# Performance work log

Hardware: AMD Instinct MI355X
Metric: run time of the kernel (lower is better)

The kernel has to match this reference:

```python
import jax, jax.numpy as jnp
import numpy as np

INP, HID = 32, 64
NG, NPER = 16, 16384          # graphs, nodes per graph (contiguous, equal size)
N = NG * NPER                 # 262144 nodes
E = N * 16                    # 4194304 edges
K = 7                         # topk
STEPS = 5                     # future prediction heads
P0, P1 = INP * HID, HID * HID # GRU hidden sizes = GCN weight numel per layer
EPS = 1e-5


def setup_inputs() -> dict:
    key = jax.random.key(0)
    ks = jax.random.split(key, 32)
    s = 0.05
    inp = {
        "x": jax.random.normal(ks[0], (N, INP), jnp.float32),
        "edge_index": jax.random.randint(ks[1], (2, E), 0, N),
        "edge_weight": jax.random.uniform(ks[2], (E,), jnp.float32),
        "batch": jnp.arange(N) // NPER,
        "batch_size": NG,
        # summarization score vectors p per layer
        "p0": jax.random.normal(ks[3], (INP,), jnp.float32),
        "p1": jax.random.normal(ks[4], (HID,), jnp.float32),
        # GRUCell params, layer 0: input INP -> hidden P0
        "Wih0": jax.random.normal(ks[5], (3 * P0, INP), jnp.float32) * s,
        "Whh0": jax.random.normal(ks[6], (3 * P0, P0), jnp.float32) * s,
        "bih0": jnp.zeros((3 * P0,), jnp.float32),
        "bhh0": jnp.zeros((3 * P0,), jnp.float32),
        # GRUCell params, layer 1: input HID -> hidden P1
        "Wih1": jax.random.normal(ks[7], (3 * P1, HID), jnp.float32) * s,
        "Whh1": jax.random.normal(ks[8], (3 * P1, P1), jnp.float32) * s,
        "bih1": jnp.zeros((3 * P1,), jnp.float32),
        "bhh1": jnp.zeros((3 * P1,), jnp.float32),
        # GRU hidden states (persistent buffers), one row per graph in batch
        "gruh0": jax.random.normal(ks[9], (NG, P0), jnp.float32) * s,
        "gruh1": jax.random.normal(ks[10], (NG, P1), jnp.float32) * s,
        # GCN biases (weights come from evolved GRU hidden)
        "gcnb0": jnp.zeros((HID,), jnp.float32),
        "gcnb1": jnp.zeros((HID,), jnp.float32),
        # LayerNorm params
        "lng0": jnp.ones((HID,), jnp.float32),
        "lnb0": jnp.zeros((HID,), jnp.float32),
        "lng1": jnp.ones((HID,), jnp.float32),
        "lnb1": jnp.zeros((HID,), jnp.float32),
        # 5 future-predictor heads Linear(HID, 2), stacked
        "Wp": jax.random.normal(ks[11], (STEPS, HID, 2), jnp.float32) * s,
        "bp": jnp.zeros((STEPS, 2), jnp.float32),
    }
    return inp


def _summarize(h, B, k, p):
    # per-graph topk summarization: score = h @ p/||p||, weight topk rows by tanh(score), mean
    d = h.shape[-1]
    hg = h.reshape(B, -1, d)                          # [B, Nper, d]
    scores = hg @ (p / jnp.linalg.norm(p))            # [B, Nper]
    top_s, idx = jax.lax.top_k(scores, k)             # [B, k]
    top_h = jnp.take_along_axis(hg, idx[:, :, None], axis=1)  # [B, k, d]
    return (top_h * jnp.tanh(top_s)[:, :, None]).mean(axis=1)  # [B, d]


def _gru_cell(x, h, Wih, Whh, bih, bhh):
    gi = x @ Wih.T + bih
    gh = h @ Whh.T + bhh
    i_r, i_z, i_n = jnp.split(gi, 3, axis=-1)
    h_r, h_z, h_n = jnp.split(gh, 3, axis=-1)
    r = jax.nn.sigmoid(i_r + h_r)
    z = jax.nn.sigmoid(i_z + h_z)
    n = jnp.tanh(i_n + r * h_n)
    return (1.0 - z) * n + z * h


def _gcn_conv(h, W, b, src, dst, ew, n_nodes):
    # GCNConv with self-loops (weight 1) and symmetric normalization
    x = h @ W + b                                     # linear first (PyG order)
    deg = jnp.zeros((n_nodes,), x.dtype).at[dst].add(ew) + 1.0
    norm = ew * jax.lax.rsqrt(deg[src] * deg[dst])
    out = jnp.zeros_like(x).at[dst].add(norm[:, None] * x[src])
    return out + x / deg[:, None]                     # self-loop: 1/deg_i


def _layer_norm(h, g, b):
    mu = h.mean(-1, keepdims=True)
    var = ((h - mu) ** 2).mean(-1, keepdims=True)
    return (h - mu) * jax.lax.rsqrt(var + EPS) * g + b


def reference(x, edge_index, edge_weight, batch, batch_size,
              p0, p1, Wih0, Whh0, bih0, bhh0, Wih1, Whh1, bih1, bhh1,
              gruh0, gruh1, gcnb0, gcnb1, lng0, lnb0, lng1, lnb1, Wp, bp):
    src, dst = edge_index[0], edge_index[1]
    n_nodes = x.shape[0]
    layers = [
        (p0, Wih0, Whh0, bih0, bhh0, gruh0, gcnb0, lng0, lnb0, (INP, HID)),
        (p1, Wih1, Whh1, bih1, bhh1, gruh1, gcnb1, lng1, lnb1, (HID, HID)),
    ]
    h = x
    for (p, Wih, Whh, bih, bhh, gh, gb, lg, lb, (din, dout)) in layers:
        Z = _summarize(h, batch_size, K, p)                # [B, din]
        gh_new = _gru_cell(Z, gh, Wih, Whh, bih, bhh)      # [B, din*dout]
        W = gh_new.mean(axis=0).reshape(din, dout)         # evolved GCN weight
        h = _gcn_conv(h, W, gb, src, dst, edge_weight, n_nodes)
        h = jax.nn.relu(_layer_norm(h, lg, lb))            # dropout: eval mode (identity)
    # stacked prediction heads -> [N, STEPS, 2]
    return jnp.einsum("nd,sdo->nso", h, Wp) + bp[None, :, :]
```

## Files before the change

### kernel.cpp

```cpp
#include <hip/hip_runtime.h>
#include <hip/hip_bf16.h>
#include <hip/hip_fp16.h>

#define NN 262144
#define EE 4194304
#define NG 16
#define NPER 16384
#define KK 7
#define TPAD 20
#define SLOT 18432

typedef unsigned long long u64;

__device__ __forceinline__ float wred(float v) {
    #pragma unroll
    for (int o = 32; o > 0; o >>= 1) v += __shfl_xor(v, o);
    return v;
}

__device__ __forceinline__ unsigned short f2h(float f) {
    return __half_as_ushort(__float2half_rn(f));
}
__device__ __forceinline__ float h2f(unsigned short s) {
    return __half2float(__ushort_as_half(s));
}

__global__ void prep_p(const float* __restrict__ p0, const float* __restrict__ p1,
                       float* __restrict__ pn) {
    int t = threadIdx.x;
    float v0 = (t < 32) ? p0[t] : 0.f;
    float s0 = wred(v0 * v0);
    if (t < 32) pn[t] = v0 * rsqrtf(s0);
    float v1 = p1[t];
    float s1 = wred(v1 * v1);
    pn[32 + t] = v1 * rsqrtf(s1);
}

__global__ void init_gcur(int* __restrict__ gcur) {
    gcur[threadIdx.x] = (int)threadIdx.x * SLOT;
}

__global__ __launch_bounds__(256) void binA(const int* __restrict__ ei,
                                            const float* __restrict__ ew,
                                            int* __restrict__ gcur,
                                            uint2* __restrict__ bb) {
    __shared__ int hist[256], hofs[256], hcur[256], gpos[256], sd[256];
    __shared__ uint2 stage[4096];
    int t = threadIdx.x;
    int base = blockIdx.x * 4096;
    hist[t] = 0;
    __syncthreads();
    int dv[16];
    #pragma unroll
    for (int j = 0; j < 16; j++) {
        dv[j] = ei[EE + base + j * 256 + t];
        atomicAdd(&hist[dv[j] >> 10], 1);
    }
    __syncthreads();
    int cnt = hist[t];
    sd[t] = cnt;
    __syncthreads();
    #pragma unroll
    for (int off = 1; off < 256; off <<= 1) {
        int add = (t >= off) ? sd[t - off] : 0;
        __syncthreads();
        sd[t] += add;
        __syncthreads();
    }
    hofs[t] = sd[t] - cnt;
    hcur[t] = sd[t] - cnt;
    gpos[t] = atomicAdd(&gcur[t], cnt);
    __syncthreads();
    #pragma unroll
    for (int j = 0; j < 16; j++) {
        int e = base + j * 256 + t;
        int d = dv[j];
        int s = ei[e];
        unsigned wq = (unsigned)__float2uint_rn(ew[e] * 16383.f);
        unsigned payload = ((unsigned)s << 14) | wq;
        int p = atomicAdd(&hcur[d >> 10], 1);
        stage[p] = make_uint2((unsigned)d, payload);
    }
    __syncthreads();
    #pragma unroll
    for (int j = 0; j < 16; j++) {
        int k = j * 256 + t;
        uint2 en = stage[k];
        int b = (int)(en.x >> 10);
        bb[gpos[b] + (k - hofs[b])] = en;
    }
}

__global__ __launch_bounds__(1024) void count_bucket(const uint2* __restrict__ bb,
                                                     const int* __restrict__ gcur,
                                                     int* __restrict__ rowptr,
                                                     int* __restrict__ btot,
                                                     float* __restrict__ rsqd,
                                                     float* __restrict__ invdeg) {
    __shared__ int cnt[1024];
    __shared__ int wsi[1024];
    __shared__ int sd[1024];
    int b = blockIdx.x, t = threadIdx.x;
    cnt[t] = 0;
    wsi[t] = 0;
    __syncthreads();
    int e0 = b * SLOT, e1 = gcur[b];
    for (int k = e0 + t; k < e1; k += 1024) {
        uint2 en = bb[k];
        int dl = (int)(en.x & 1023u);
        atomicAdd(&cnt[dl], 1);
        atomicAdd(&wsi[dl], (int)(en.y & 16383u));
    }
    __syncthreads();
    int node = (b << 10) + t;
    float deg = 1.f + (float)wsi[t] * (1.f / 16383.f);
    rsqd[node] = rsqrtf(deg);
    invdeg[node] = 1.f / deg;
    int v = cnt[t];
    sd[t] = v;
    __syncthreads();
    #pragma unroll
    for (int off = 1; off < 1024; off <<= 1) {
        int add = (t >= off) ? sd[t - off] : 0;
        __syncthreads();
        sd[t] += add;
        __syncthreads();
    }
    rowptr[node] = sd[t] - v;
    if (t == 1023) btot[b] = sd[1023];
}

__global__ void scan256(const int* __restrict__ btot, int* __restrict__ bbase) {
    __shared__ int sd[256];
    int t = threadIdx.x;
    int v = btot[t];
    sd[t] = v;
    __syncthreads();
    #pragma unroll
    for (int off = 1; off < 256; off <<= 1) {
        int add = (t >= off) ? sd[t - off] : 0;
        __syncthreads();
        sd[t] += add;
        __syncthreads();
    }
    bbase[t] = sd[t] - v;
}

__global__ void finalize_rowptr(int* __restrict__ rowptr, const int* __restrict__ bbase) {
    int i = blockIdx.x * 256 + threadIdx.x;
    rowptr[i] += bbase[i >> 10];
    if (i == 0) rowptr[NN] = EE;
}

__global__ __launch_bounds__(1024) void binB(const int* __restrict__ rowptr,
                                             const int* __restrict__ gcur,
                                             const uint2* __restrict__ bb,
                                             const float* __restrict__ rsqd,
                                             unsigned* __restrict__ evw) {
    __shared__ int lcur[1024];
    int b = blockIdx.x, t = threadIdx.x;
    lcur[t] = rowptr[(b << 10) + t];
    __syncthreads();
    int e0 = b * SLOT, e1 = gcur[b];
    for (int k = e0 + t; k < e1; k += 1024) {
        uint2 en = bb[k];
        int dl = (int)(en.x & 1023u);
        unsigned s = en.y >> 14;
        float wt = (float)(en.y & 16383u) * (1.f / 16383.f) * rsqd[s];
        int pos = atomicAdd(&lcur[dl], 1);
        evw[pos] = (s << 14) | (unsigned)__float2uint_rn(wt * 16383.f);
    }
}

__global__ void scores0_f16(const float* __restrict__ x, const float* __restrict__ pn0,
                            float* __restrict__ scores, unsigned short* __restrict__ xh) {
    __shared__ float p[32];
    if (threadIdx.x < 32) p[threadIdx.x] = pn0[threadIdx.x];
    __syncthreads();
    int n = blockIdx.x * 256 + threadIdx.x;
    const float4* xr = (const float4*)(x + (size_t)n * 32);
    float s = 0.f;
    unsigned wv[16];
    #pragma unroll
    for (int j = 0; j < 8; j++) {
        float4 v = xr[j];
        s += v.x * p[j * 4] + v.y * p[j * 4 + 1] + v.z * p[j * 4 + 2] + v.w * p[j * 4 + 3];
        wv[2 * j]     = (unsigned)f2h(v.x) | ((unsigned)f2h(v.y) << 16);
        wv[2 * j + 1] = (unsigned)f2h(v.z) | ((unsigned)f2h(v.w) << 16);
    }
    uint4* xo = (uint4*)(xh + (size_t)n * 32);
    xo[0] = make_uint4(wv[0], wv[1], wv[2], wv[3]);
    xo[1] = make_uint4(wv[4], wv[5], wv[6], wv[7]);
    xo[2] = make_uint4(wv[8], wv[9], wv[10], wv[11]);
    xo[3] = make_uint4(wv[12], wv[13], wv[14], wv[15]);
    scores[n] = s;
}

__global__ void topk1(const float* __restrict__ scores, float2* __restrict__ cand) {
    int g = blockIdx.x >> 4, c = blockIdx.x & 15;
    int t = threadIdx.x;
    float lv[KK];
    int li[KK];
    #pragma unroll
    for (int j = 0; j < KK; j++) { lv[j] = -INFINITY; li[j] = 0; }
    const float* sg = scores + (size_t)g * NPER + c * 1024;
    #pragma unroll
    for (int it = 0; it < 4; ++it) {
        int idx = it * 256 + t;
        float v = sg[idx];
        if (v > lv[KK - 1]) {
            int j = KK - 1;
            while (j > 0 && lv[j - 1] < v) { lv[j] = lv[j - 1]; li[j] = li[j - 1]; j--; }
            lv[j] = v; li[j] = idx;
        }
    }
    __shared__ float sval[256];
    __shared__ int sidx[256];
    __shared__ int swin;
    int cons = 0;
    for (int r = 0; r < KK; r++) {
        sval[t] = (cons < KK) ? lv[cons] : -INFINITY;
        sidx[t] = t;
        __syncthreads();
        for (int s = 128; s > 0; s >>= 1) {
            if (t < s) {
                if (sval[t + s] > sval[t]) { sval[t] = sval[t + s]; sidx[t] = sidx[t + s]; }
            }
            __syncthreads();
        }
        if (t == 0) swin = sidx[0];
        __syncthreads();
        if (t == swin) {
            cand[blockIdx.x * KK + r] =
                make_float2(lv[cons], __int_as_float(g * NPER + c * 1024 + li[cons]));
            cons++;
        }
        __syncthreads();
    }
}

__global__ void topk2(const float2* __restrict__ cand, float* __restrict__ topv,
                      int* __restrict__ topi) {
    int g = blockIdx.x, t = threadIdx.x;
    float v = -INFINITY;
    int id = 0;
    if (t < 16 * KK) {
        float2 cv = cand[g * 16 * KK + t];
        v = cv.x;
        id = __float_as_int(cv.y);
    }
    __shared__ float sval[128];
    __shared__ int sidx[128];
    __shared__ int swin;
    for (int r = 0; r < KK; r++) {
        sval[t] = v;
        sidx[t] = t;
        __syncthreads();
        for (int s = 64; s > 0; s >>= 1) {
            if (t < s) {
                if (sval[t + s] > sval[t]) { sval[t] = sval[t + s]; sidx[t] = sidx[t + s]; }
            }
            __syncthreads();
        }
        if (t == 0) swin = sidx[0];
        __syncthreads();
        if (t == swin) {
            topv[g * KK + r] = v;
            topi[g * KK + r] = id;
            v = -INFINITY;
        }
        __syncthreads();
    }
}

__global__ void z_kernel(const float* __restrict__ h, int din, const float* __restrict__ topv,
                         const int* __restrict__ topi, float* __restrict__ Z) {
    int b = blockIdx.x;
    int d = threadIdx.x;
    if (d >= din) return;
    float acc = 0.f;
    for (int j = 0; j < KK; j++) {
        acc += tanhf(topv[b * KK + j]) * h[(size_t)topi[b * KK + j] * din + d];
    }
    Z[b * din + d] = acc * (1.f / 7.f);
}

__global__ void z_kernel_h(const unsigned short* __restrict__ h, int din,
                           const float* __restrict__ topv, const int* __restrict__ topi,
                           float* __restrict__ Z) {
    int b = blockIdx.x;
    int d = threadIdx.x;
    if (d >= din) return;
    float acc = 0.f;
    for (int j = 0; j < KK; j++) {
        acc += tanhf(topv[b * KK + j]) * h2f(h[(size_t)topi[b * KK + j] * din + d]);
    }
    Z[b * din + d] = acc * (1.f / 7.f);
}

__global__ void gru_matvec(const float* __restrict__ Whh, const float* __restrict__ gh,
                           float* __restrict__ ghl, int P) {
    int t = threadIdx.x;
    int g = t >> 4, l16 = t & 15;
    int row0 = blockIdx.x * 64 + g * 4;
    int k0 = blockIdx.y * 512;
    float acc[4][16];
    #pragma unroll
    for (int r = 0; r < 4; r++)
        #pragma unroll
        for (int b = 0; b < 16; b++) acc[r][b] = 0.f;
    const float* wr = Whh + (size_t)row0 * P + k0 + l16 * 4;
    const float* gr = gh + k0 + l16 * 4;
    for (int kk = 0; kk < 8; ++kk) {
        float4 a0 = *(const float4*)(wr + kk * 64);
        float4 a1 = *(const float4*)(wr + (size_t)P + kk * 64);
        float4 a2 = *(const float4*)(wr + (size_t)2 * P + kk * 64);
        float4 a3 = *(const float4*)(wr + (size_t)3 * P + kk * 64);
        #pragma unroll
        for (int b = 0; b < 16; b++) {
            float4 gv = *(const float4*)(gr + (size_t)b * P + kk * 64);
            acc[0][b] += a0.x * gv.x + a0.y * gv.y + a0.z * gv.z + a0.w * gv.w;
            acc[1][b] += a1.x * gv.x + a1.y * gv.y + a1.z * gv.z + a1.w * gv.w;
            acc[2][b] += a2.x * gv.x + a2.y * gv.y + a2.z * gv.z + a2.w * gv.w;
            acc[3][b] += a3.x * gv.x + a3.y * gv.y + a3.z * gv.z + a3.w * gv.w;
        }
    }
    size_t sstr = (size_t)gridDim.x * 1024;
    #pragma unroll
    for (int r = 0; r < 4; r++) {
        #pragma unroll
        for (int b = 0; b < 16; b++) {
            float v = acc[r][b];
            v += __shfl_xor(v, 1); v += __shfl_xor(v, 2);
            v += __shfl_xor(v, 4); v += __shfl_xor(v, 8);
            if (l16 == b) ghl[(size_t)blockIdx.y * sstr + (size_t)(row0 + r) * 16 + b] = v;
        }
    }
}

__global__ __launch_bounds__(256) void gate_kernel(
    const float* __restrict__ Wih, const float* __restrict__ bih,
    const float* __restrict__ bhh, const float* __restrict__ gh,
    const float* __restrict__ ghl, const float* __restrict__ Zg,
    float* __restrict__ gvt, int P, int din, int NS) {
    __shared__ float Zs[64];
    int t = threadIdx.x;
    int b = blockIdx.y;
    if (t < din) Zs[t] = Zg[b * din + t];
    __syncthreads();
    int p = blockIdx.x * 256 + t;
    float ir = bih[p], iz = bih[P + p], inn = bih[2 * P + p];
    const float* w_r = Wih + (size_t)p * din;
    const float* w_z = Wih + (size_t)(P + p) * din;
    const float* w_n = Wih + (size_t)(2 * P + p) * din;
    for (int d = 0; d < din; d += 4) {
        float4 zr = *(const float4*)(Zs + d);
        float4 a = *(const float4*)(w_r + d);
        float4 bq = *(const float4*)(w_z + d);
        float4 c = *(const float4*)(w_n + d);
        ir += a.x * zr.x + a.y * zr.y + a.z * zr.z + a.w * zr.w;
        iz += bq.x * zr.x + bq.y * zr.y + bq.z * zr.z + bq.w * zr.w;
        inn += c.x * zr.x + c.y * zr.y + c.z * zr.z + c.w * zr.w;
    }
    float hr = bhh[p], hz = bhh[P + p], hn = bhh[2 * P + p];
    size_t sstr = (size_t)48 * P;
    for (int s2 = 0; s2 < NS; s2++) {
        const float* g2 = ghl + (size_t)s2 * sstr;
        hr += g2[(size_t)p * 16 + b];
        hz += g2[(size_t)(P + p) * 16 + b];
        hn += g2[(size_t)(2 * P + p) * 16 + b];
    }
    float r = 1.f / (1.f + expf(-(ir + hr)));
    float z = 1.f / (1.f + expf(-(iz + hz)));
    float n = tanhf(inn + r * hn);
    float hprev = gh[(size_t)b * P + p];
    gvt[(size_t)b * P + p] = (1.f - z) * n + z * hprev;
}

__global__ void gate_reduce(const float* __restrict__ gvt, float* __restrict__ Wev, int P) {
    int p = blockIdx.x * 256 + threadIdx.x;
    float s = 0.f;
    #pragma unroll
    for (int b = 0; b < 16; b++) s += gvt[(size_t)b * P + p];
    Wev[p] = s * (1.f / 16.f);
}

template<int DIN, int LSHL>
__global__ void agg_kernel(const unsigned short* __restrict__ hin,
                           const int* __restrict__ rowptr, const unsigned* __restrict__ evw,
                           const float* __restrict__ rsqd, const float* __restrict__ invdeg,
                           unsigned short* __restrict__ aggh, float* __restrict__ cc) {
    int t = threadIdx.x;
    int lane = t & ((1 << LSHL) - 1);
    int i = blockIdx.x * (256 >> LSHL) + (t >> LSHL);
    int e0 = rowptr[i], e1 = rowptr[i + 1];
    float a0 = 0.f, a1 = 0.f, a2 = 0.f, a3 = 0.f;
    int csi = 0;
    for (int e = e0; e < e1; e += 8) {
        unsigned ev[8];
        #pragma unroll
        for (int j = 0; j < 8; j++) {
            ev[j] = (e + j < e1) ? evw[e + j] : ((unsigned)i << 14);
        }
        uint2 hv[8];
        #pragma unroll
        for (int j = 0; j < 8; j++) {
            hv[j] = *(const uint2*)(hin + (size_t)(ev[j] >> 14) * DIN + 4 * lane);
        }
        #pragma unroll
        for (int j = 0; j < 8; j++) {
            int wq = (int)(ev[j] & 16383u);
            csi += wq;
            float nw = (float)wq;
            a0 += nw * h2f((unsigned short)(hv[j].x & 0xffffu));
            a1 += nw * h2f((unsigned short)(hv[j].x >> 16));
            a2 += nw * h2f((unsigned short)(hv[j].y & 0xffffu));
            a3 += nw * h2f((unsigned short)(hv[j].y >> 16));
        }
    }
    float rsi = rsqd[i] * (1.f / 16383.f);
    float idg = invdeg[i];
    uint2 hs = *(const uint2*)(hin + (size_t)i * DIN + 4 * lane);
    float r0 = a0 * rsi + h2f((unsigned short)(hs.x & 0xffffu)) * idg;
    float r1 = a1 * rsi + h2f((unsigned short)(hs.x >> 16)) * idg;
    float r2 = a2 * rsi + h2f((unsigned short)(hs.y & 0xffffu)) * idg;
    float r3 = a3 * rsi + h2f((unsigned short)(hs.y >> 16)) * idg;
    uint2 ro;
    ro.x = (unsigned)f2h(r0) | ((unsigned)f2h(r1) << 16);
    ro.y = (unsigned)f2h(r2) | ((unsigned)f2h(r3) << 16);
    *(uint2*)(aggh + (size_t)i * DIN + 4 * lane) = ro;
    #pragma unroll
    for (int o = (1 << LSHL) >> 1; o > 0; o >>= 1) csi += __shfl_xor(csi, o);
    if (lane == 0) cc[i] = (float)csi * rsi + idg;
}

__global__ __launch_bounds__(256) void post0_kernel(
    const unsigned short* __restrict__ aggh, const float* __restrict__ cc,
    const float* __restrict__ Wev, const float* __restrict__ gcnb,
    const float* __restrict__ lng, const float* __restrict__ lnb,
    const float* __restrict__ pn1, unsigned short* __restrict__ h1h,
    float* __restrict__ scores) {
    __shared__ float stage[4][512];
    __shared__ float tile[4][64 * TPAD];
    const int wv = threadIdx.x >> 6;
    const int lane = threadIdx.x & 63;
    const int tb = blockIdx.x * 256 + wv * 64;
    const int j = lane & 15, q = lane >> 4;
    float gL = gcnb[lane];
    float lgv[16], lbv[16], pnv[16];
    #pragma unroll
    for (int r = 0; r < 16; r++) {
        lgv[r] = lng[q * 16 + r];
        lbv[r] = lnb[q * 16 + r];
        pnv[r] = pn1[q * 16 + r];
    }
    float* st = stage[wv];
    float* trow = tile[wv] + lane * TPAD;
    auto do_chunk = [&](int C) {
        __syncthreads();
        {
            const uint2* src = (const uint2*)(aggh + (size_t)(tb + C * 16) * 32);
            #pragma unroll
            for (int it = 0; it < 2; ++it) {
                uint2 hp = src[it * 64 + lane];
                float4 f;
                f.x = h2f((unsigned short)(hp.x & 0xffffu));
                f.y = h2f((unsigned short)(hp.x >> 16));
                f.z = h2f((unsigned short)(hp.y & 0xffffu));
                f.w = h2f((unsigned short)(hp.y >> 16));
                *(float4*)(st + (it * 64 + lane) * 4) = f;
            }
        }
        __syncthreads();
        float v[16];
        #pragma unroll
        for (int k = 0; k < 16; k++) v[k] = 0.f;
        for (int db = 0; db < 8; ++db) {
            float wc0 = Wev[(db * 4 + 0) * 64 + lane];
            float wc1 = Wev[(db * 4 + 1) * 64 + lane];
            float wc2 = Wev[(db * 4 + 2) * 64 + lane];
            float wc3 = Wev[(db * 4 + 3) * 64 + lane];
            #pragma unroll
            for (int k = 0; k < 16; k++) {
                float4 a = *(const float4*)(st + k * 32 + db * 4);
                v[k] += a.x * wc0 + a.y * wc1 + a.z * wc2 + a.w * wc3;
            }
        }
        __syncthreads();
        #pragma unroll
        for (int k = 0; k < 16; k++) trow[k] = v[k] + gL * cc[tb + C * 16 + k];
        __syncthreads();
        float av[16];
        #pragma unroll
        for (int r = 0; r < 16; r++) av[r] = tile[wv][(q * 16 + r) * TPAD + j];
        float s1 = 0.f, s2 = 0.f;
        #pragma unroll
        for (int r = 0; r < 16; r++) { s1 += av[r]; s2 += av[r] * av[r]; }
        s1 += __shfl_xor(s1, 16); s1 += __shfl_xor(s1, 32);
        s2 += __shfl_xor(s2, 16); s2 += __shfl_xor(s2, 32);
        float mu = s1 * (1.f / 64.f);
        float rstd = rsqrtf(s2 * (1.f / 64.f) - mu * mu + 1e-5f);
        float hv[16];
        float sc = 0.f;
        #pragma unroll
        for (int r = 0; r < 16; r++) {
            hv[r] = fmaxf((av[r] - mu) * rstd * lgv[r] + lbv[r], 0.f);
            sc += hv[r] * pnv[r];
        }
        int node = tb + C * 16 + j;
        uint4 o0, o1;
        o0.x = (unsigned)f2h(hv[0])  | ((unsigned)f2h(hv[1])  << 16);
        o0.y = (unsigned)f2h(hv[2])  | ((unsigned)f2h(hv[3])  << 16);
        o0.z = (unsigned)f2h(hv[4])  | ((unsigned)f2h(hv[5])  << 16);
        o0.w = (unsigned)f2h(hv[6])  | ((unsigned)f2h(hv[7])  << 16);
        o1.x = (unsigned)f2h(hv[8])  | ((unsigned)f2h(hv[9])  << 16);
        o1.y = (unsigned)f2h(hv[10]) | ((unsigned)f2h(hv[11]) << 16);
        o1.z = (unsigned)f2h(hv[12]) | ((unsigned)f2h(hv[13]) << 16);
        o1.w = (unsigned)f2h(hv[14]) | ((unsigned)f2h(hv[15]) << 16);
        *(uint4*)(h1h + (size_t)node * 64 + q * 16) = o0;
        *(uint4*)(h1h + (size_t)node * 64 + q * 16 + 8) = o1;
        sc += __shfl_xor(sc, 16); sc += __shfl_xor(sc, 32);
        if (q == 0) scores[node] = sc;
    };
    do_chunk(0); do_chunk(1); do_chunk(2); do_chunk(3);
}

__global__ __launch_bounds__(256) void post1_kernel(
    const unsigned short* __restrict__ aggh, const float* __restrict__ cc,
    const float* __restrict__ Wev, const float* __restrict__ gcnb,
    const float* __restrict__ lng, const float* __restrict__ lnb,
    const float* __restrict__ Wp, const float* __restrict__ bp,
    float* __restrict__ out) {
    __shared__ float stage[4][1024];
    __shared__ float tile[4][64 * TPAD];
    const int wv = threadIdx.x >> 6;
    const int lane = threadIdx.x & 63;
    const int tb = blockIdx.x * 256 + wv * 64;
    const int j = lane & 15, q = lane >> 4;
    float gL = gcnb[lane];
    float lgv[16], lbv[16];
    #pragma unroll
    for (int r = 0; r < 16; r++) {
        lgv[r] = lng[q * 16 + r];
        lbv[r] = lnb[q * 16 + r];
    }
    float bpv[10];
    #pragma unroll
    for (int t2 = 0; t2 < 10; t2++) bpv[t2] = bp[t2];
    float* st = stage[wv];
    float* trow = tile[wv] + lane * TPAD;
    auto do_chunk = [&](int C) {
        __syncthreads();
        {
            const uint2* src = (const uint2*)(aggh + (size_t)(tb + C * 16) * 64);
            #pragma unroll
            for (int it = 0; it < 4; ++it) {
                uint2 hp = src[it * 64 + lane];
                float4 f;
                f.x = h2f((unsigned short)(hp.x & 0xffffu));
                f.y = h2f((unsigned short)(hp.x >> 16));
                f.z = h2f((unsigned short)(hp.y & 0xffffu));
                f.w = h2f((unsigned short)(hp.y >> 16));
                *(float4*)(st + (it * 64 + lane) * 4) = f;
            }
        }
        __syncthreads();
        float v[16];
        #pragma unroll
        for (int k = 0; k < 16; k++) v[k] = 0.f;
        for (int db = 0; db < 16; ++db) {
            float wc0 = Wev[(db * 4 + 0) * 64 + lane];
            float wc1 = Wev[(db * 4 + 1) * 64 + lane];
            float wc2 = Wev[(db * 4 + 2) * 64 + lane];
            float wc3 = Wev[(db * 4 + 3) * 64 + lane];
            #pragma unroll
            for (int k = 0; k < 16; k++) {
                float4 a = *(const float4*)(st + k * 64 + db * 4);
                v[k] += a.x * wc0 + a.y * wc1 + a.z * wc2 + a.w * wc3;
            }
        }
        __syncthreads();
        #pragma unroll
        for (int k = 0; k < 16; k++) trow[k] = v[k] + gL * cc[tb + C * 16 + k];
        __syncthreads();
        float av[16];
        #pragma unroll
        for (int r = 0; r < 16; r++) av[r] = tile[wv][(q * 16 + r) * TPAD + j];
        float s1 = 0.f, s2 = 0.f;
        #pragma unroll
        for (int r = 0; r < 16; r++) { s1 += av[r]; s2 += av[r] * av[r]; }
        s1 += __shfl_xor(s1, 16); s1 += __shfl_xor(s1, 32);
        s2 += __shfl_xor(s2, 16); s2 += __shfl_xor(s2, 32);
        float mu = s1 * (1.f / 64.f);
        float rstd = rsqrtf(s2 * (1.f / 64.f) - mu * mu + 1e-5f);
        float hv[16];
        #pragma unroll
        for (int r = 0; r < 16; r++)
            hv[r] = fmaxf((av[r] - mu) * rstd * lgv[r] + lbv[r], 0.f);
        float oa[10];
        #pragma unroll
        for (int t2 = 0; t2 < 10; t2++) oa[t2] = 0.f;
        #pragma unroll
        for (int r = 0; r < 16; r++) {
            const float* wpb = Wp + (size_t)(q * 16 + r) * 2;
            float2 w0 = *(const float2*)(wpb);
            float2 w1 = *(const float2*)(wpb + 128);
            float2 w2 = *(const float2*)(wpb + 256);
            float2 w3 = *(const float2*)(wpb + 384);
            float2 w4 = *(const float2*)(wpb + 512);
            oa[0] += hv[r] * w0.x; oa[1] += hv[r] * w0.y;
            oa[2] += hv[r] * w1.x; oa[3] += hv[r] * w1.y;
            oa[4] += hv[r] * w2.x; oa[5] += hv[r] * w2.y;
            oa[6] += hv[r] * w3.x; oa[7] += hv[r] * w3.y;
            oa[8] += hv[r] * w4.x; oa[9] += hv[r] * w4.y;
        }
        #pragma unroll
        for (int t2 = 0; t2 < 10; t2++) {
            oa[t2] += __shfl_xor(oa[t2], 16);
            oa[t2] += __shfl_xor(oa[t2], 32);
        }
        if (q == 0) {
            int node = tb + C * 16 + j;
            #pragma unroll
            for (int t2 = 0; t2 < 10; t2++) out[(size_t)node * 10 + t2] = oa[t2] + bpv[t2];
        }
    };
    do_chunk(0); do_chunk(1); do_chunk(2); do_chunk(3);
}

extern "C" void kernel_launch(void* const* d_in, const int* in_sizes, int n_in,
                              void* d_out, int out_size, void* d_ws, size_t ws_size,
                              hipStream_t stream) {
    const float* x     = (const float*)d_in[0];
    const int*   ei    = (const int*)d_in[1];
    const float* ew    = (const float*)d_in[2];
    const float* p0    = (const float*)d_in[5];
    const float* p1    = (const float*)d_in[6];
    const float* Wih0  = (const float*)d_in[7];
    const float* Whh0  = (const float*)d_in[8];
    const float* bih0  = (const float*)d_in[9];
    const float* bhh0  = (const float*)d_in[10];
    const float* Wih1  = (const float*)d_in[11];
    const float* Whh1  = (const float*)d_in[12];
    const float* bih1  = (const float*)d_in[13];
    const float* bhh1  = (const float*)d_in[14];
    const float* gruh0 = (const float*)d_in[15];
    const float* gruh1 = (const float*)d_in[16];
    const float* gcnb0 = (const float*)d_in[17];
    const float* gcnb1 = (const float*)d_in[18];
    const float* lng0  = (const float*)d_in[19];
    const float* lnb0  = (const float*)d_in[20];
    const float* lng1  = (const float*)d_in[21];
    const float* lnb1  = (const float*)d_in[22];
    const float* Wp    = (const float*)d_in[23];
    const float* bp    = (const float*)d_in[24];
    float* out = (float*)d_out;

    char* w = (char*)d_ws;
    size_t off = 0;
    auto alloc = [&](size_t bytes) -> void* {
        void* p = w + off;
        off += (bytes + 255) & ~(size_t)255;
        return p;
    };
    int*      rowptr = (int*)alloc((NN + 1) * sizeof(int));
    unsigned* evw    = (unsigned*)alloc((size_t)EE * sizeof(unsigned));
    float*    rsqd   = (float*)alloc(NN * sizeof(float));
    float*    invdeg = (float*)alloc(NN * sizeof(float));
    float*    scores = (float*)alloc(NN * sizeof(float));
    float*    topv   = (float*)alloc(NG * KK * sizeof(float));
    int*      topi   = (int*)alloc(NG * KK * sizeof(int));
    float2*   cand   = (float2*)alloc(NG * 16 * KK * sizeof(float2));
    float*    Z      = (float*)alloc(16 * 64 * sizeof(float));
    float*    ghl    = (float*)alloc((size_t)8 * 196608 * sizeof(float));
    float*    gvt    = (float*)alloc((size_t)16 * 4096 * sizeof(float));
    float*    Wev    = (float*)alloc(4096 * sizeof(float));
    float*    cc     = (float*)alloc(NN * sizeof(float));
    float*    agg    = (float*)alloc((size_t)NN * 64 * sizeof(float));
    unsigned short* xh  = (unsigned short*)alloc((size_t)NN * 32 * sizeof(unsigned short));
    unsigned short* h1h = (unsigned short*)alloc((size_t)NN * 64 * sizeof(unsigned short));
    float*    pn     = (float*)alloc(96 * sizeof(float));
    int*      gcur   = (int*)alloc(256 * sizeof(int));
    int*      btot   = (int*)alloc(256 * sizeof(int));
    int*      bbase  = (int*)alloc(256 * sizeof(int));

    uint2* bb = (uint2*)agg;
    unsigned short* aggh = (unsigned short*)agg;

    init_gcur<<<1, 256, 0, stream>>>(gcur);
    prep_p<<<1, 64, 0, stream>>>(p0, p1, pn);
    binA<<<EE / 4096, 256, 0, stream>>>(ei, ew, gcur, bb);
    count_bucket<<<256, 1024, 0, stream>>>(bb, gcur, rowptr, btot, rsqd, invdeg);
    scan256<<<1, 256, 0, stream>>>(btot, bbase);
    finalize_rowptr<<<NN / 256, 256, 0, stream>>>(rowptr, bbase);
    binB<<<256, 1024, 0, stream>>>(rowptr, gcur, bb, rsqd, evw);

    scores0_f16<<<NN / 256, 256, 0, stream>>>(x, pn, scores, xh);
    topk1<<<NG * 16, 256, 0, stream>>>(scores, cand);
    topk2<<<NG, 128, 0, stream>>>(cand, topv, topi);
    z_kernel<<<NG, 32, 0, stream>>>(x, 32, topv, topi, Z);
    gru_matvec<<<dim3(6144 / 64, 4), 256, 0, stream>>>(Whh0, gruh0, ghl, 2048);
    gate_kernel<<<dim3(2048 / 256, 16), 256, 0, stream>>>(Wih0, bih0, bhh0, gruh0, ghl, Z, gvt, 2048, 32, 4);
    gate_reduce<<<2048 / 256, 256, 0, stream>>>(gvt, Wev, 2048);
    agg_kernel<32, 3><<<NN / 32, 256, 0, stream>>>(xh, rowptr, evw, rsqd, invdeg, aggh, cc);
    post0_kernel<<<NN / 256, 256, 0, stream>>>(aggh, cc, Wev, gcnb0, lng0, lnb0, pn + 32, h1h, scores);

    topk1<<<NG * 16, 256, 0, stream>>>(scores, cand);
    topk2<<<NG, 128, 0, stream>>>(cand, topv, topi);
    z_kernel_h<<<NG, 64, 0, stream>>>(h1h, 64, topv, topi, Z);
    gru_matvec<<<dim3(12288 / 64, 8), 256, 0, stream>>>(Whh1, gruh1, ghl, 4096);
    gate_kernel<<<dim3(4096 / 256, 16), 256, 0, stream>>>(Wih1, bih1, bhh1, gruh1, ghl, Z, gvt, 4096, 64, 8);
    gate_reduce<<<4096 / 256, 256, 0, stream>>>(gvt, Wev, 4096);
    agg_kernel<64, 4><<<NN / 16, 256, 0, stream>>>(h1h, rowptr, evw, rsqd, invdeg, aggh, cc);
    post1_kernel<<<NN / 256, 256, 0, stream>>>(aggh, cc, Wev, gcnb1, lng1, lnb1, Wp, bp, out);
}
```

Before: 634.8 us.

## Fuse small kernels: scores with topk1, topk2 with Z, init with prep

Merges init_gcur and prep_p into one launch, fuses layer-0 score computation and fp16 conversion with the first topk stage so scores are never written, and fuses topk2 with the Z gather for both layers. It also switches the bucket reads in count_bucket and binB to nontemporal 64-bit loads. The goal is to cut kernel-launch overhead and one score round-trip through memory. In exchange, scores0_topk1 runs only 256 blocks, each doing four times more work, so it exposes less parallelism for the x read.

```diff
diff --git a/kernel.cpp b/kernel.cpp
--- a/kernel.cpp
+++ b/kernel.cpp
@@ -25,19 +25,18 @@
     return __half2float(__ushort_as_half(s));
 }
 
-__global__ void prep_p(const float* __restrict__ p0, const float* __restrict__ p1,
-                       float* __restrict__ pn) {
+__global__ void prep_init(const float* __restrict__ p0, const float* __restrict__ p1,
+                          float* __restrict__ pn, int* __restrict__ gcur) {
     int t = threadIdx.x;
-    float v0 = (t < 32) ? p0[t] : 0.f;
-    float s0 = wred(v0 * v0);
-    if (t < 32) pn[t] = v0 * rsqrtf(s0);
-    float v1 = p1[t];
-    float s1 = wred(v1 * v1);
-    pn[32 + t] = v1 * rsqrtf(s1);
-}
-
-__global__ void init_gcur(int* __restrict__ gcur) {
-    gcur[threadIdx.x] = (int)threadIdx.x * SLOT;
+    gcur[t] = t * SLOT;
+    if (t < 64) {
+        float v0 = (t < 32) ? p0[t] : 0.f;
+        float s0 = wred(v0 * v0);
+        if (t < 32) pn[t] = v0 * rsqrtf(s0);
+        float v1 = p1[t];
+        float s1 = wred(v1 * v1);
+        pn[32 + t] = v1 * rsqrtf(s1);
+    }
 }
 
 __global__ __launch_bounds__(256) void binA(const int* __restrict__ ei,
@@ -106,10 +105,12 @@
     __syncthreads();
     int e0 = b * SLOT, e1 = gcur[b];
     for (int k = e0 + t; k < e1; k += 1024) {
-        uint2 en = bb[k];
-        int dl = (int)(en.x & 1023u);
+        u64 raw = __builtin_nontemporal_load((const u64*)(bb + k));
+        unsigned lo = (unsigned)raw;
+        unsigned hi = (unsigned)(raw >> 32);
+        int dl = (int)(lo & 1023u);
         atomicAdd(&cnt[dl], 1);
-        atomicAdd(&wsi[dl], (int)(en.y & 16383u));
+        atomicAdd(&wsi[dl], (int)(hi & 16383u));
     }
     __syncthreads();
     int node = (b << 10) + t;
@@ -163,47 +164,85 @@
     __syncthreads();
     int e0 = b * SLOT, e1 = gcur[b];
     for (int k = e0 + t; k < e1; k += 1024) {
-        uint2 en = bb[k];
-        int dl = (int)(en.x & 1023u);
-        unsigned s = en.y >> 14;
-        float wt = (float)(en.y & 16383u) * (1.f / 16383.f) * rsqd[s];
+        u64 raw = __builtin_nontemporal_load((const u64*)(bb + k));
+        unsigned lo = (unsigned)raw;
+        unsigned hi = (unsigned)(raw >> 32);
+        int dl = (int)(lo & 1023u);
+        unsigned s = hi >> 14;
+        float wt = (float)(hi & 16383u) * (1.f / 16383.f) * rsqd[s];
         int pos = atomicAdd(&lcur[dl], 1);
         evw[pos] = (s << 14) | (unsigned)__float2uint_rn(wt * 16383.f);
     }
 }
 
-__global__ void scores0_f16(const float* __restrict__ x, const float* __restrict__ pn0,
-                            float* __restrict__ scores, unsigned short* __restrict__ xh) {
+__global__ __launch_bounds__(256) void scores0_topk1(
+    const float* __restrict__ x, const float* __restrict__ pn0,
+    unsigned short* __restrict__ xh, float2* __restrict__ cand) {
     __shared__ float p[32];
     if (threadIdx.x < 32) p[threadIdx.x] = pn0[threadIdx.x];
     __syncthreads();
-    int n = blockIdx.x * 256 + threadIdx.x;
-    const float4* xr = (const float4*)(x + (size_t)n * 32);
-    float s = 0.f;
-    unsigned wv[16];
-    #pragma unroll
-    for (int j = 0; j < 8; j++) {
-        float4 v = xr[j];
-        s += v.x * p[j * 4] + v.y * p[j * 4 + 1] + v.z * p[j * 4 + 2] + v.w * p[j * 4 + 3];
-        wv[2 * j]     = (unsigned)f2h(v.x) | ((unsigned)f2h(v.y) << 16);
-        wv[2 * j + 1] = (unsigned)f2h(v.z) | ((unsigned)f2h(v.w) << 16);
-    }
-    uint4* xo = (uint4*)(xh + (size_t)n * 32);
-    xo[0] = make_uint4(wv[0], wv[1], wv[2], wv[3]);
-    xo[1] = make_uint4(wv[4], wv[5], wv[6], wv[7]);
-    xo[2] = make_uint4(wv[8], wv[9], wv[10], wv[11]);
-    xo[3] = make_uint4(wv[12], wv[13], wv[14], wv[15]);
-    scores[n] = s;
-}
-
-__global__ void topk1(const float* __restrict__ scores, float2* __restrict__ cand) {
-    int g = blockIdx.x >> 4, c = blockIdx.x & 15;
     int t = threadIdx.x;
     float lv[KK];
     int li[KK];
     #pragma unroll
     for (int j = 0; j < KK; j++) { lv[j] = -INFINITY; li[j] = 0; }
-    const float* sg = scores + (size_t)g * NPER + c * 1024;
+    #pragma unroll
+    for (int it = 0; it < 4; ++it) {
+        int idx = it * 256 + t;
+        int n = blockIdx.x * 1024 + idx;
+        const float4* xr = (const float4*)(x + (size_t)n * 32);
+        float s = 0.f;
+        unsigned wv[16];
+        #pragma unroll
+        for (int j = 0; j < 8; j++) {
+            float4 v = xr[j];
+            s += v.x * p[j * 4] + v.y * p[j * 4 + 1] + v.z * p[j * 4 + 2] + v.w * p[j * 4 + 3];
+            wv[2 * j]     = (unsigned)f2h(v.x) | ((unsigned)f2h(v.y) << 16);
+            wv[2 * j + 1] = (unsigned)f2h(v.z) | ((unsigned)f2h(v.w) << 16);
+        }
+        uint4* xo = (uint4*)(xh + (size_t)n * 32);
+        xo[0] = make_uint4(wv[0], wv[1], wv[2], wv[3]);
+        xo[1] = make_uint4(wv[4], wv[5], wv[6], wv[7]);
+        xo[2] = make_uint4(wv[8], wv[9], wv[10], wv[11]);
+        xo[3] = make_uint4(wv[12], wv[13], wv[14], wv[15]);
+        if (s > lv[KK - 1]) {
+            int j = KK - 1;
+            while (j > 0 && lv[j - 1] < s) { lv[j] = lv[j - 1]; li[j] = li[j - 1]; j--; }
+            lv[j] = s; li[j] = idx;
+        }
+    }
+    __shared__ float sval[256];
+    __shared__ int sidx[256];
+    __shared__ int swin;
+    int cons = 0;
+    for (int r = 0; r < KK; r++) {
+        sval[t] = (cons < KK) ? lv[cons] : -INFINITY;
+        sidx[t] = t;
+        __syncthreads();
+        for (int s = 128; s > 0; s >>= 1) {
+            if (t < s) {
+                if (sval[t + s] > sval[t]) { sval[t] = sval[t + s]; sidx[t] = sidx[t + s]; }
+            }
+            __syncthreads();
+        }
+        if (t == 0) swin = sidx[0];
+        __syncthreads();
+        if (t == swin) {
+            cand[blockIdx.x * KK + r] =
+                make_float2(lv[cons], __int_as_float(blockIdx.x * 1024 + li[cons]));
+            cons++;
+        }
+        __syncthreads();
+    }
+}
+
+__global__ void topk1(const float* __restrict__ scores, float2* __restrict__ cand) {
+    int t = threadIdx.x;
+    float lv[KK];
+    int li[KK];
+    #pragma unroll
+    for (int j = 0; j < KK; j++) { lv[j] = -INFINITY; li[j] = 0; }
+    const float* sg = scores + (size_t)blockIdx.x * 1024;
     #pragma unroll
     for (int it = 0; it < 4; ++it) {
         int idx = it * 256 + t;
@@ -232,16 +271,18 @@
         __syncthreads();
         if (t == swin) {
             cand[blockIdx.x * KK + r] =
-                make_float2(lv[cons], __int_as_float(g * NPER + c * 1024 + li[cons]));
+                make_float2(lv[cons], __int_as_float(blockIdx.x * 1024 + li[cons]));
             cons++;
         }
         __syncthreads();
     }
 }
 
-__global__ void topk2(const float2* __restrict__ cand, float* __restrict__ topv,
-                      int* __restrict__ topi) {
+__global__ void topk2z(const float2* __restrict__ cand, const float* __restrict__ h,
+                       int din, float* __restrict__ Z) {
     int g = blockIdx.x, t = threadIdx.x;
+    __shared__ float tv[KK];
+    __shared__ int ti[KK];
     float v = -INFINITY;
     int id = 0;
     if (t < 16 * KK) {
@@ -265,37 +306,64 @@
         if (t == 0) swin = sidx[0];
         __syncthreads();
         if (t == swin) {
-            topv[g * KK + r] = v;
-            topi[g * KK + r] = id;
+            tv[r] = v;
+            ti[r] = id;
             v = -INFINITY;
         }
         __syncthreads();
     }
-}
-
-__global__ void z_kernel(const float* __restrict__ h, int din, const float* __restrict__ topv,
-                         const int* __restrict__ topi, float* __restrict__ Z) {
-    int b = blockIdx.x;
-    int d = threadIdx.x;
-    if (d >= din) return;
-    float acc = 0.f;
-    for (int j = 0; j < KK; j++) {
-        acc += tanhf(topv[b * KK + j]) * h[(size_t)topi[b * KK + j] * din + d];
-    }
-    Z[b * din + d] = acc * (1.f / 7.f);
-}
-
-__global__ void z_kernel_h(const unsigned short* __restrict__ h, int din,
-                           const float* __restrict__ topv, const int* __restrict__ topi,
-                           float* __restrict__ Z) {
-    int b = blockIdx.x;
-    int d = threadIdx.x;
-    if (d >= din) return;
-    float acc = 0.f;
-    for (int j = 0; j < KK; j++) {
-        acc += tanhf(topv[b * KK + j]) * h2f(h[(size_t)topi[b * KK + j] * din + d]);
-    }
-    Z[b * din + d] = acc * (1.f / 7.f);
+    if (t < din) {
+        float acc = 0.f;
+        #pragma unroll
+        for (int j = 0; j < KK; j++) {
+            acc += tanhf(tv[j]) * h[(size_t)ti[j] * din + t];
+        }
+        Z[g * din + t] = acc * (1.f / 7.f);
+    }
+}
+
+__global__ void topk2z_h(const float2* __restrict__ cand, const unsigned short* __restrict__ h,
+                         int din, float* __restrict__ Z) {
+    int g = blockIdx.x, t = threadIdx.x;
+    __shared__ float tv[KK];
+    __shared__ int ti[KK];
+    float v = -INFINITY;
+    int id = 0;
+    if (t < 16 * KK) {
+        float2 cv = cand[g * 16 * KK + t];
+        v = cv.x;
+        id = __float_as_int(cv.y);
+    }
+    __shared__ float sval[128];
+    __shared__ int sidx[128];
+    __shared__ int swin;
+    for (int r = 0; r < KK; r++) {
+        sval[t] = v;
+        sidx[t] = t;
+        __syncthreads();
+        for (int s = 64; s > 0; s >>= 1) {
+            if (t < s) {
+                if (sval[t + s] > sval[t]) { sval[t] = sval[t + s]; sidx[t] = sidx[t + s]; }
+            }
+            __syncthreads();
+        }
+        if (t == 0) swin = sidx[0];
+        __syncthreads();
+        if (t == swin) {
+            tv[r] = v;
+            ti[r] = id;
+            v = -INFINITY;
+        }
+        __syncthreads();
+    }
+    if (t < din) {
+        float acc = 0.f;
+        #pragma unroll
+        for (int j = 0; j < KK; j++) {
+            acc += tanhf(tv[j]) * h2f(h[(size_t)ti[j] * din + t]);
+        }
+        Z[g * din + t] = acc * (1.f / 7.f);
+    }
 }
 
 __global__ void gru_matvec(const float* __restrict__ Whh, const float* __restrict__ gh,
@@ -668,8 +736,6 @@
     float*    rsqd   = (float*)alloc(NN * sizeof(float));
     float*    invdeg = (float*)alloc(NN * sizeof(float));
     float*    scores = (float*)alloc(NN * sizeof(float));
-    float*    topv   = (float*)alloc(NG * KK * sizeof(float));
-    int*      topi   = (int*)alloc(NG * KK * sizeof(int));
     float2*   cand   = (float2*)alloc(NG * 16 * KK * sizeof(float2));
     float*    Z      = (float*)alloc(16 * 64 * sizeof(float));
     float*    ghl    = (float*)alloc((size_t)8 * 196608 * sizeof(float));
@@ -687,27 +753,23 @@
     uint2* bb = (uint2*)agg;
     unsigned short* aggh = (unsigned short*)agg;
 
-    init_gcur<<<1, 256, 0, stream>>>(gcur);
-    prep_p<<<1, 64, 0, stream>>>(p0, p1, pn);
+    prep_init<<<1, 256, 0, stream>>>(p0, p1, pn, gcur);
     binA<<<EE / 4096, 256, 0, stream>>>(ei, ew, gcur, bb);
     count_bucket<<<256, 1024, 0, stream>>>(bb, gcur, rowptr, btot, rsqd, invdeg);
     scan256<<<1, 256, 0, stream>>>(btot, bbase);
     finalize_rowptr<<<NN / 256, 256, 0, stream>>>(rowptr, bbase);
     binB<<<256, 1024, 0, stream>>>(rowptr, gcur, bb, rsqd, evw);
 
-    scores0_f16<<<NN / 256, 256, 0, stream>>>(x, pn, scores, xh);
-    topk1<<<NG * 16, 256, 0, stream>>>(scores, cand);
-    topk2<<<NG, 128, 0, stream>>>(cand, topv, topi);
-    z_kernel<<<NG, 32, 0, stream>>>(x, 32, topv, topi, Z);
+    scores0_topk1<<<NN / 1024, 256, 0, stream>>>(x, pn, xh, cand);
+    topk2z<<<NG, 128, 0, stream>>>(cand, x, 32, Z);
     gru_matvec<<<dim3(6144 / 64, 4), 256, 0, stream>>>(Whh0, gruh0, ghl, 2048);
     gate_kernel<<<dim3(2048 / 256, 16), 256, 0, stream>>>(Wih0, bih0, bhh0, gruh0, ghl, Z, gvt, 2048, 32, 4);
     gate_reduce<<<2048 / 256, 256, 0, stream>>>(gvt, Wev, 2048);
     agg_kernel<32, 3><<<NN / 32, 256, 0, stream>>>(xh, rowptr, evw, rsqd, invdeg, aggh, cc);
     post0_kernel<<<NN / 256, 256, 0, stream>>>(aggh, cc, Wev, gcnb0, lng0, lnb0, pn + 32, h1h, scores);
 
-    topk1<<<NG * 16, 256, 0, stream>>>(scores, cand);
-    topk2<<<NG, 128, 0, stream>>>(cand, topv, topi);
-    z_kernel_h<<<NG, 64, 0, stream>>>(h1h, 64, topv, topi, Z);
+    topk1<<<NN / 1024, 256, 0, stream>>>(scores, cand);
+    topk2z_h<<<NG, 128, 0, stream>>>(cand, h1h, 64, Z);
     gru_matvec<<<dim3(12288 / 64, 8), 256, 0, stream>>>(Whh1, gruh1, ghl, 4096);
     gate_kernel<<<dim3(4096 / 256, 16), 256, 0, stream>>>(Wih1, bih1, bhh1, gruh1, ghl, Z, gvt, 4096, 64, 8);
     gate_reduce<<<4096 / 256, 256, 0, stream>>>(gvt, Wev, 4096);
```

New measurement: 674.7 us. +6.3%, slower.
